# Kernel tuning notes

Measured on AMD Instinct MI355X. Metric: run time of the kernel, lower is better.

## Reference

```python
import jax, jax.numpy as jnp
import numpy as np

BH, L, D = 32, 2048, 64  # (batch*heads), seq_len, d_k

def setup_inputs() -> dict:
    key = jax.random.key(0)
    kq, kk, kv = jax.random.split(key, 3)
    q = jax.random.normal(kq, (BH, L, D), dtype=jnp.float32)
    k = jax.random.normal(kk, (BH, L, D), dtype=jnp.float32)
    v = jax.random.normal(kv, (BH, L, D), dtype=jnp.float32)
    # causal mask: True = masked (future positions), broadcast to all heads
    causal = jnp.triu(jnp.ones((L, L), dtype=jnp.bool_), k=1)
    mask = jnp.broadcast_to(causal, (BH, L, L))
    return {"q": q, "k": k, "v": v, "mask": mask}

def reference(q, k, v, mask):
    # attn = softmax(q @ k^T / sqrt(d_k)) with masked positions set to -inf;
    # dropout is identity in eval mode.
    scale = 1.0 / np.sqrt(D).astype(np.float32)
    scores = jnp.einsum('bld,bmd->blm', q, k) * scale  # (BH, L, L)
    scores = jnp.where(mask, -jnp.inf, scores)
    p = jax.nn.softmax(scores, axis=-1)
    return jnp.einsum('blm,bmd->bld', p, v)  # (BH, L, D)
```

## Files before the change

kernel.cpp:

```cpp
#include <hip/hip_runtime.h>
#include <hip/hip_bf16.h>


#define LEN 2048
#define DD  64
#define BQ  128
#define BK  64
#define NQT (LEN / BQ)
#define NKT (LEN / BK)
#define TSHORTS 9216
#define TBYTES  18432

typedef short s16x8 __attribute__((ext_vector_type(8)));
typedef float f32x4 __attribute__((ext_vector_type(4)));

__device__ __forceinline__ short bfbits(float f) {
  union { float f; unsigned u; } a; a.f = f;
  unsigned u = a.u;
  u += 0x7fffu + ((u >> 16) & 1u);
  return (short)(u >> 16);
}

#define SCL (0.125f * 1.44269504088896f)

__global__ __launch_bounds__(256, 4)
void prep(const float* __restrict__ Q, const float* __restrict__ K,
          const float* __restrict__ V, short* __restrict__ KVp,
          short* __restrict__ Qb)
{
  const int b = blockIdx.x, t = threadIdx.x;
  if (b < 2048) {
    const int idx = (b * 256 + t) * 8;
    const float4 a = *(const float4*)(Q + idx);
    const float4 c = *(const float4*)(Q + idx + 4);
    s16x8 o;
    o[0] = bfbits(a.x * SCL); o[1] = bfbits(a.y * SCL);
    o[2] = bfbits(a.z * SCL); o[3] = bfbits(a.w * SCL);
    o[4] = bfbits(c.x * SCL); o[5] = bfbits(c.y * SCL);
    o[6] = bfbits(c.z * SCL); o[7] = bfbits(c.w * SCL);
    *(s16x8*)(Qb + idx) = o;
  } else if (b < 2048 + 2304) {
    const int u = (b - 2048) * 256 + t;
    const int chunk = u % 9;
    const int ru = u / 9;
    const int row = ru & 63;
    const int ht  = ru >> 6;
    short* dst = KVp + (size_t)ht * TSHORTS + row * 72 + chunk * 8;
    s16x8 o = {0, 0, 0, 0, 0, 0, 0, 0};
    if (chunk < 8) {
      const float* src = K + ((size_t)ht * 64 + row) * 64 + chunk * 8;
      const float4 a = *(const float4*)src;
      const float4 c = *(const float4*)(src + 4);
      o[0] = bfbits(a.x); o[1] = bfbits(a.y); o[2] = bfbits(a.z); o[3] = bfbits(a.w);
      o[4] = bfbits(c.x); o[5] = bfbits(c.y); o[6] = bfbits(c.z); o[7] = bfbits(c.w);
    }
    *(s16x8*)dst = o;
  } else {
    const int u = (b - (2048 + 2304)) * 256 + t;
    const int d = u & 63;
    const int rest = u >> 6;
    const int chunk = rest % 9;
    const int ht = rest / 9;
    short* dst = KVp + (size_t)ht * TSHORTS + 4608 + d * 72 + chunk * 8;
    s16x8 o = {0, 0, 0, 0, 0, 0, 0, 0};
    if (chunk < 8) {
      const float* src = V + (size_t)ht * 4096 + (size_t)chunk * 8 * 64 + d;
      #pragma unroll
      for (int j = 0; j < 8; ++j) o[j] = bfbits(src[j * 64]);
    }
    *(s16x8*)dst = o;
  }
}

__device__ __forceinline__ void ld16(const void* g, void* l) {
  __builtin_amdgcn_global_load_lds(
      (const __attribute__((address_space(1))) unsigned int*)g,
      (__attribute__((address_space(3))) unsigned int*)l, 16, 0, 0);
}

__global__ __launch_bounds__(512, 4)
void fattn(const short* __restrict__ KVp, const short* __restrict__ Qb,
           float* __restrict__ Og)
{
  __shared__ __align__(16) short kv_lds[TSHORTS];
  __shared__ __align__(16) short pb[8][16][72];

  const int bx = blockIdx.x;
  const int bh = bx & 31;
  const int qt = (NQT - 1) - (bx >> 5);
  const int q0 = qt * BQ;
  const int tid = threadIdx.x;
  const int wave = tid >> 6, lane = tid & 63;
  const int lq = lane & 15, quad = lane >> 4;
  const int rowb = q0 + wave * 16;

  s16x8 qf[2];
  {
    const short* qrow = Qb + ((size_t)bh * LEN + rowb + lq) * DD;
    qf[0] = *(const s16x8*)(qrow + quad * 8);
    qf[1] = *(const s16x8*)(qrow + 32 + quad * 8);
  }

  f32x4 o[4];
  float l[4];
  #pragma unroll
  for (int nt = 0; nt < 4; ++nt) o[nt] = (f32x4){0.f, 0.f, 0.f, 0.f};
  #pragma unroll
  for (int r = 0; r < 4; ++r) l[r] = 0.f;

  const char* gtiles = (const char*)(KVp + (size_t)bh * NKT * TSHORTS);
  const int ntiles = 2 * qt + 2;

  for (int it = 0; it < ntiles; ++it) {
    __syncthreads();
    {
      const char* g = gtiles + (size_t)it * TBYTES;
      char* ldst = (char*)kv_lds;
      const int o0 = wave * 1024 + lane * 16;
      ld16(g + o0, ldst + o0);
      ld16(g + o0 + 8192, ldst + o0 + 8192);
      if (wave < 2) ld16(g + o0 + 16384, ldst + o0 + 16384);
    }
    __syncthreads();

    const int k0 = it * BK;
    if (k0 <= rowb + 15) {
      f32x4 s[4];
      #pragma unroll
      for (int nt = 0; nt < 4; ++nt) {
        f32x4 acc = (f32x4){0.f, 0.f, 0.f, 0.f};
        #pragma unroll
        for (int c = 0; c < 2; ++c) {
          const s16x8 kf = *(const s16x8*)&kv_lds[(nt * 16 + lq) * 72 + c * 32 + quad * 8];
          acc = __builtin_amdgcn_mfma_f32_16x16x32_bf16(qf[c], kf, acc, 0, 0, 0);
        }
        s[nt] = acc;
      }

      if (k0 + BK - 1 > rowb) {
        #pragma unroll
        for (int nt = 0; nt < 4; ++nt) {
          const int col = k0 + nt * 16 + lq;
          #pragma unroll
          for (int r = 0; r < 4; ++r)
            if (col > rowb + quad * 4 + r) s[nt][r] = -1e30f;
        }
      }

      #pragma unroll
      for (int nt = 0; nt < 4; ++nt)
        #pragma unroll
        for (int r = 0; r < 4; ++r)
          s[nt][r] = exp2f(s[nt][r]);
      #pragma unroll
      for (int r = 0; r < 4; ++r)
        l[r] += (s[0][r] + s[1][r]) + (s[2][r] + s[3][r]);

      #pragma unroll
      for (int nt = 0; nt < 4; ++nt)
        #pragma unroll
        for (int r = 0; r < 4; ++r)
          pb[wave][quad * 4 + r][nt * 16 + lq] = bfbits(s[nt][r]);
      s16x8 pf0 = *(const s16x8*)&pb[wave][lq][quad * 8];
      s16x8 pf1 = *(const s16x8*)&pb[wave][lq][32 + quad * 8];

      #pragma unroll
      for (int nt = 0; nt < 4; ++nt) {
        const s16x8 vf0 = *(const s16x8*)&kv_lds[4608 + (nt * 16 + lq) * 72 + quad * 8];
        const s16x8 vf1 = *(const s16x8*)&kv_lds[4608 + (nt * 16 + lq) * 72 + 32 + quad * 8];
        o[nt] = __builtin_amdgcn_mfma_f32_16x16x32_bf16(pf0, vf0, o[nt], 0, 0, 0);
        o[nt] = __builtin_amdgcn_mfma_f32_16x16x32_bf16(pf1, vf1, o[nt], 0, 0, 0);
      }
    }
  }

  #pragma unroll
  for (int r = 0; r < 4; ++r) {
    float rs = l[r];
    rs += __shfl_xor(rs, 1, 64);
    rs += __shfl_xor(rs, 2, 64);
    rs += __shfl_xor(rs, 4, 64);
    rs += __shfl_xor(rs, 8, 64);
    const float inv = 1.0f / rs;
    float* orow = Og + ((size_t)bh * LEN + rowb + quad * 4 + r) * DD;
    #pragma unroll
    for (int nt = 0; nt < 4; ++nt)
      orow[nt * 16 + lq] = o[nt][r] * inv;
  }
}

extern "C" void kernel_launch(void* const* d_in, const int* in_sizes, int n_in,
                              void* d_out, int out_size, void* d_ws, size_t ws_size,
                              hipStream_t stream) {
  (void)in_sizes; (void)n_in; (void)out_size; (void)ws_size;
  const float* q = (const float*)d_in[0];
  const float* k = (const float*)d_in[1];
  const float* v = (const float*)d_in[2];
  float* out = (float*)d_out;

  short* KVp = (short*)d_ws;
  short* Qb  = (short*)((char*)d_ws + (size_t)1024 * TBYTES);

  prep<<<dim3(2048 + 2304 + 2304), dim3(256), 0, stream>>>(q, k, v, KVp, Qb);
  fattn<<<dim3(32 * NQT), dim3(512), 0, stream>>>(KVp, Qb, out);
}
```

Before: 659.7 us.

## Double-buffer KV tiles, fuse Q conversion into attention, and halve block waves

The attention kernel now double-buffers KV tiles in LDS, issuing the next tile's async global-to-LDS copy before computing on the current one. This removes one barrier per iteration and overlaps loads with MFMA work. Q conversion to bf16 moves from the prep kernel into the attention kernel, and each block uses 4 waves that each handle 32 query rows (two 16-row blocks), which changes occupancy to 3 blocks per CU. Other changes: q-tiles are scheduled so heavy and light causal tiles interleave, exp2 uses the hardware builtin, and P is rounded with a cheaper bf16 rounding that is not ties-to-even. Prep drops the zero-filled padding chunks.

```diff
diff --git a/kernel.cpp b/kernel.cpp
--- a/kernel.cpp
+++ b/kernel.cpp
@@ -6,8 +6,8 @@
 #define DD  64
 #define BQ  128
 #define BK  64
-#define NQT (LEN / BQ)
-#define NKT (LEN / BK)
+#define NQT 16
+#define NKT 32
 #define TSHORTS 9216
 #define TBYTES  18432
 
@@ -24,51 +24,32 @@
 #define SCL (0.125f * 1.44269504088896f)
 
 __global__ __launch_bounds__(256, 4)
-void prep(const float* __restrict__ Q, const float* __restrict__ K,
-          const float* __restrict__ V, short* __restrict__ KVp,
-          short* __restrict__ Qb)
+void prep(const float* __restrict__ K, const float* __restrict__ V,
+          short* __restrict__ KVp)
 {
   const int b = blockIdx.x, t = threadIdx.x;
   if (b < 2048) {
-    const int idx = (b * 256 + t) * 8;
-    const float4 a = *(const float4*)(Q + idx);
-    const float4 c = *(const float4*)(Q + idx + 4);
+    const int u = b * 256 + t;
+    const int chunk = u & 7;
+    const int row = (u >> 3) & 63;
+    const int ht  = u >> 9;
+    const float* src = K + ((size_t)ht * 64 + row) * 64 + chunk * 8;
+    const float4 a = *(const float4*)src;
+    const float4 c = *(const float4*)(src + 4);
     s16x8 o;
-    o[0] = bfbits(a.x * SCL); o[1] = bfbits(a.y * SCL);
-    o[2] = bfbits(a.z * SCL); o[3] = bfbits(a.w * SCL);
-    o[4] = bfbits(c.x * SCL); o[5] = bfbits(c.y * SCL);
-    o[6] = bfbits(c.z * SCL); o[7] = bfbits(c.w * SCL);
-    *(s16x8*)(Qb + idx) = o;
-  } else if (b < 2048 + 2304) {
+    o[0] = bfbits(a.x); o[1] = bfbits(a.y); o[2] = bfbits(a.z); o[3] = bfbits(a.w);
+    o[4] = bfbits(c.x); o[5] = bfbits(c.y); o[6] = bfbits(c.z); o[7] = bfbits(c.w);
+    *(s16x8*)(KVp + (size_t)ht * TSHORTS + row * 72 + chunk * 8) = o;
+  } else {
     const int u = (b - 2048) * 256 + t;
-    const int chunk = u % 9;
-    const int ru = u / 9;
-    const int row = ru & 63;
-    const int ht  = ru >> 6;
-    short* dst = KVp + (size_t)ht * TSHORTS + row * 72 + chunk * 8;
-    s16x8 o = {0, 0, 0, 0, 0, 0, 0, 0};
-    if (chunk < 8) {
-      const float* src = K + ((size_t)ht * 64 + row) * 64 + chunk * 8;
-      const float4 a = *(const float4*)src;
-      const float4 c = *(const float4*)(src + 4);
-      o[0] = bfbits(a.x); o[1] = bfbits(a.y); o[2] = bfbits(a.z); o[3] = bfbits(a.w);
-      o[4] = bfbits(c.x); o[5] = bfbits(c.y); o[6] = bfbits(c.z); o[7] = bfbits(c.w);
-    }
-    *(s16x8*)dst = o;
-  } else {
-    const int u = (b - (2048 + 2304)) * 256 + t;
     const int d = u & 63;
-    const int rest = u >> 6;
-    const int chunk = rest % 9;
-    const int ht = rest / 9;
-    short* dst = KVp + (size_t)ht * TSHORTS + 4608 + d * 72 + chunk * 8;
-    s16x8 o = {0, 0, 0, 0, 0, 0, 0, 0};
-    if (chunk < 8) {
-      const float* src = V + (size_t)ht * 4096 + (size_t)chunk * 8 * 64 + d;
-      #pragma unroll
-      for (int j = 0; j < 8; ++j) o[j] = bfbits(src[j * 64]);
-    }
-    *(s16x8*)dst = o;
+    const int chunk = (u >> 6) & 7;
+    const int ht = u >> 9;
+    const float* src = V + (size_t)ht * 4096 + (size_t)chunk * 8 * 64 + d;
+    s16x8 o;
+    #pragma unroll
+    for (int j = 0; j < 8; ++j) o[j] = bfbits(src[j * 64]);
+    *(s16x8*)(KVp + (size_t)ht * TSHORTS + 4608 + d * 72 + chunk * 8) = o;
   }
 }
 
@@ -78,61 +59,87 @@
       (__attribute__((address_space(3))) unsigned int*)l, 16, 0, 0);
 }
 
-__global__ __launch_bounds__(512, 4)
-void fattn(const short* __restrict__ KVp, const short* __restrict__ Qb,
+__device__ __forceinline__ void stage18k(const char* g, char* l,
+                                         int wave, int lane) {
+  const int o0 = wave * 1024 + lane * 16;
+  ld16(g + o0,          l + o0);
+  ld16(g + o0 + 4096,   l + o0 + 4096);
+  ld16(g + o0 + 8192,   l + o0 + 8192);
+  ld16(g + o0 + 12288,  l + o0 + 12288);
+  if (wave < 2) ld16(g + o0 + 16384, l + o0 + 16384);
+}
+
+__global__ __launch_bounds__(256, 3)
+void fattn(const short* __restrict__ KVp, const float* __restrict__ Qg,
            float* __restrict__ Og)
 {
-  __shared__ __align__(16) short kv_lds[TSHORTS];
-  __shared__ __align__(16) short pb[8][16][72];
+  __shared__ __align__(16) short kv2[2][TSHORTS];
+  __shared__ __align__(16) short pb[4][16][72];
 
   const int bx = blockIdx.x;
   const int bh = bx & 31;
-  const int qt = (NQT - 1) - (bx >> 5);
+  const int g  = bx >> 5;
+  const int qt = (g < 8) ? (15 - g) : (g - 8);
   const int q0 = qt * BQ;
   const int tid = threadIdx.x;
   const int wave = tid >> 6, lane = tid & 63;
   const int lq = lane & 15, quad = lane >> 4;
-  const int rowb = q0 + wave * 16;
-
-  s16x8 qf[2];
-  {
-    const short* qrow = Qb + ((size_t)bh * LEN + rowb + lq) * DD;
-    qf[0] = *(const s16x8*)(qrow + quad * 8);
-    qf[1] = *(const s16x8*)(qrow + 32 + quad * 8);
-  }
-
-  f32x4 o[4];
-  float l[4];
-  #pragma unroll
-  for (int nt = 0; nt < 4; ++nt) o[nt] = (f32x4){0.f, 0.f, 0.f, 0.f};
-  #pragma unroll
-  for (int r = 0; r < 4; ++r) l[r] = 0.f;
+  const int rowb0 = q0 + wave * 32;
 
   const char* gtiles = (const char*)(KVp + (size_t)bh * NKT * TSHORTS);
   const int ntiles = 2 * qt + 2;
 
+  stage18k(gtiles, (char*)kv2[0], wave, lane);
+
+  s16x8 qf[2][2];
+  #pragma unroll
+  for (int rb = 0; rb < 2; ++rb) {
+    const float* qrow = Qg + ((size_t)bh * LEN + rowb0 + rb * 16 + lq) * DD;
+    #pragma unroll
+    for (int c = 0; c < 2; ++c) {
+      const float4 a = *(const float4*)(qrow + c * 32 + quad * 8);
+      const float4 b = *(const float4*)(qrow + c * 32 + quad * 8 + 4);
+      s16x8 t;
+      t[0] = bfbits(a.x * SCL); t[1] = bfbits(a.y * SCL);
+      t[2] = bfbits(a.z * SCL); t[3] = bfbits(a.w * SCL);
+      t[4] = bfbits(b.x * SCL); t[5] = bfbits(b.y * SCL);
+      t[6] = bfbits(b.z * SCL); t[7] = bfbits(b.w * SCL);
+      qf[rb][c] = t;
+    }
+  }
+
+  f32x4 o[2][4];
+  float l[2][4];
+  #pragma unroll
+  for (int rb = 0; rb < 2; ++rb) {
+    #pragma unroll
+    for (int nt = 0; nt < 4; ++nt) o[rb][nt] = (f32x4){0.f, 0.f, 0.f, 0.f};
+    #pragma unroll
+    for (int r = 0; r < 4; ++r) l[rb][r] = 0.f;
+  }
+
   for (int it = 0; it < ntiles; ++it) {
     __syncthreads();
-    {
-      const char* g = gtiles + (size_t)it * TBYTES;
-      char* ldst = (char*)kv_lds;
-      const int o0 = wave * 1024 + lane * 16;
-      ld16(g + o0, ldst + o0);
-      ld16(g + o0 + 8192, ldst + o0 + 8192);
-      if (wave < 2) ld16(g + o0 + 16384, ldst + o0 + 16384);
-    }
-    __syncthreads();
-
+    if (it + 1 < ntiles)
+      stage18k(gtiles + (size_t)(it + 1) * TBYTES,
+               (char*)kv2[(it + 1) & 1], wave, lane);
+
+    const short* kb = kv2[it & 1];
     const int k0 = it * BK;
-    if (k0 <= rowb + 15) {
+
+    #pragma unroll
+    for (int rb = 0; rb < 2; ++rb) {
+      const int rowb = rowb0 + rb * 16;
+      if (k0 > rowb + 15) continue;
+
       f32x4 s[4];
       #pragma unroll
       for (int nt = 0; nt < 4; ++nt) {
         f32x4 acc = (f32x4){0.f, 0.f, 0.f, 0.f};
         #pragma unroll
         for (int c = 0; c < 2; ++c) {
-          const s16x8 kf = *(const s16x8*)&kv_lds[(nt * 16 + lq) * 72 + c * 32 + quad * 8];
-          acc = __builtin_amdgcn_mfma_f32_16x16x32_bf16(qf[c], kf, acc, 0, 0, 0);
+          const s16x8 kf = *(const s16x8*)&kb[(nt * 16 + lq) * 72 + c * 32 + quad * 8];
+          acc = __builtin_amdgcn_mfma_f32_16x16x32_bf16(qf[rb][c], kf, acc, 0, 0, 0);
         }
         s[nt] = acc;
       }
@@ -151,41 +158,46 @@
       for (int nt = 0; nt < 4; ++nt)
         #pragma unroll
         for (int r = 0; r < 4; ++r)
-          s[nt][r] = exp2f(s[nt][r]);
+          s[nt][r] = __builtin_amdgcn_exp2f(s[nt][r]);
       #pragma unroll
       for (int r = 0; r < 4; ++r)
-        l[r] += (s[0][r] + s[1][r]) + (s[2][r] + s[3][r]);
+        l[rb][r] += (s[0][r] + s[1][r]) + (s[2][r] + s[3][r]);
 
       #pragma unroll
       for (int nt = 0; nt < 4; ++nt)
         #pragma unroll
-        for (int r = 0; r < 4; ++r)
-          pb[wave][quad * 4 + r][nt * 16 + lq] = bfbits(s[nt][r]);
-      s16x8 pf0 = *(const s16x8*)&pb[wave][lq][quad * 8];
-      s16x8 pf1 = *(const s16x8*)&pb[wave][lq][32 + quad * 8];
+        for (int r = 0; r < 4; ++r) {
+          union { float f; unsigned u; } cv; cv.f = s[nt][r];
+          pb[wave][quad * 4 + r][nt * 16 + lq] = (short)((cv.u + 0x8000u) >> 16);
+        }
+      const s16x8 pf0 = *(const s16x8*)&pb[wave][lq][quad * 8];
+      const s16x8 pf1 = *(const s16x8*)&pb[wave][lq][32 + quad * 8];
 
       #pragma unroll
       for (int nt = 0; nt < 4; ++nt) {
-        const s16x8 vf0 = *(const s16x8*)&kv_lds[4608 + (nt * 16 + lq) * 72 + quad * 8];
-        const s16x8 vf1 = *(const s16x8*)&kv_lds[4608 + (nt * 16 + lq) * 72 + 32 + quad * 8];
-        o[nt] = __builtin_amdgcn_mfma_f32_16x16x32_bf16(pf0, vf0, o[nt], 0, 0, 0);
-        o[nt] = __builtin_amdgcn_mfma_f32_16x16x32_bf16(pf1, vf1, o[nt], 0, 0, 0);
+        const s16x8 vf0 = *(const s16x8*)&kb[4608 + (nt * 16 + lq) * 72 + quad * 8];
+        const s16x8 vf1 = *(const s16x8*)&kb[4608 + (nt * 16 + lq) * 72 + 32 + quad * 8];
+        o[rb][nt] = __builtin_amdgcn_mfma_f32_16x16x32_bf16(pf0, vf0, o[rb][nt], 0, 0, 0);
+        o[rb][nt] = __builtin_amdgcn_mfma_f32_16x16x32_bf16(pf1, vf1, o[rb][nt], 0, 0, 0);
       }
     }
   }
 
   #pragma unroll
-  for (int r = 0; r < 4; ++r) {
-    float rs = l[r];
-    rs += __shfl_xor(rs, 1, 64);
-    rs += __shfl_xor(rs, 2, 64);
-    rs += __shfl_xor(rs, 4, 64);
-    rs += __shfl_xor(rs, 8, 64);
-    const float inv = 1.0f / rs;
-    float* orow = Og + ((size_t)bh * LEN + rowb + quad * 4 + r) * DD;
-    #pragma unroll
-    for (int nt = 0; nt < 4; ++nt)
-      orow[nt * 16 + lq] = o[nt][r] * inv;
+  for (int rb = 0; rb < 2; ++rb) {
+    #pragma unroll
+    for (int r = 0; r < 4; ++r) {
+      float rs = l[rb][r];
+      rs += __shfl_xor(rs, 1, 64);
+      rs += __shfl_xor(rs, 2, 64);
+      rs += __shfl_xor(rs, 4, 64);
+      rs += __shfl_xor(rs, 8, 64);
+      const float inv = 1.0f / rs;
+      float* orow = Og + ((size_t)bh * LEN + rowb0 + rb * 16 + quad * 4 + r) * DD;
+      #pragma unroll
+      for (int nt = 0; nt < 4; ++nt)
+        orow[nt * 16 + lq] = o[rb][nt][r] * inv;
+    }
   }
 }
 
@@ -199,8 +211,7 @@
   float* out = (float*)d_out;
 
   short* KVp = (short*)d_ws;
-  short* Qb  = (short*)((char*)d_ws + (size_t)1024 * TBYTES);
-
-  prep<<<dim3(2048 + 2304 + 2304), dim3(256), 0, stream>>>(q, k, v, KVp, Qb);
-  fattn<<<dim3(32 * NQT), dim3(512), 0, stream>>>(KVp, Qb, out);
-}
+
+  prep<<<dim3(4096), dim3(256), 0, stream>>>(k, v, KVp);
+  fattn<<<dim3(32 * NQT), dim3(256), 0, stream>>>(KVp, q, out);
+}
```

Result: no change. 654.5 us (-0.8%).
